# Performance work log

Hardware: AMD Instinct MI355X
Metric: run time of the kernel (lower is better)

## Reference

```python
import jax, jax.numpy as jnp
import numpy as np

N_NODES = 100000
N_EDGES = 3200000
IN_SIZE = 256
HID_SIZE = 256
OUT_SIZE = 64


def setup_inputs() -> dict:
    key = jax.random.key(0)
    ks = jax.random.split(key, 8)
    X = jax.random.normal(ks[0], (N_NODES, IN_SIZE), dtype=jnp.float32)
    edge_vals = jax.random.uniform(ks[1], (N_EDGES,), dtype=jnp.float32)
    # xavier-uniform-ish init for weights
    lim1 = float(np.sqrt(6.0 / (IN_SIZE + HID_SIZE)))
    W1 = jax.random.uniform(ks[2], (IN_SIZE, HID_SIZE), minval=-lim1, maxval=lim1, dtype=jnp.float32)
    b1 = jnp.zeros((HID_SIZE,), dtype=jnp.float32)
    lim2 = float(np.sqrt(6.0 / (HID_SIZE + OUT_SIZE)))
    W2 = jax.random.uniform(ks[3], (HID_SIZE, OUT_SIZE), minval=-lim2, maxval=lim2, dtype=jnp.float32)
    b2 = jnp.zeros((OUT_SIZE,), dtype=jnp.float32)
    row = jnp.sort(jax.random.randint(ks[4], (N_EDGES,), 0, N_NODES, dtype=jnp.int32))
    col = jax.random.randint(ks[5], (N_EDGES,), 0, N_NODES, dtype=jnp.int32)
    return {"X": X, "edge_vals": edge_vals, "W1": W1, "b1": b1,
            "W2": W2, "b2": b2, "row": row, "col": col}


def reference(X, edge_vals, W1, b1, W2, b2, row, col):
    """2-layer GCN (eval mode, dropout = identity).

    A is a sparse NxN matrix in COO form: A[row[e], col[e]] = edge_vals[e].
    Layer: relu(A @ (X @ W1) + b1); output: A @ (h @ W2) + b2.
    """
    n = X.shape[0]

    def spmm(dense):  # (A @ dense): gather columns, scale, segment-sum over rows
        gathered = edge_vals[:, None] * dense[col]        # [E, F]
        return jax.ops.segment_sum(gathered, row, num_segments=n)

    h = spmm(X @ W1) + b1          # [N, HID]
    h = jax.nn.relu(h)
    out = spmm(h @ W2) + b2        # [N, OUT]
    return out
```

## Files before the change

kernel.cpp:

```cpp
#include <hip/hip_runtime.h>


constexpr int IN_SIZE = 256;
constexpr int HID = 256;
constexpr int OUTF = 64;

typedef __bf16 bf16x8 __attribute__((ext_vector_type(8)));
typedef float f32x4 __attribute__((ext_vector_type(4)));

__device__ __forceinline__ ushort f2b(float f) {
    uint u = __float_as_uint(f);
    uint r = (u + 0x7fffu + ((u >> 16) & 1u)) >> 16;
    return (ushort)r;
}

__device__ __forceinline__ void fma4(float* a, uint word, float w) {
    a[0] += w * (float)(word & 0xffu);
    a[1] += w * (float)((word >> 8) & 0xffu);
    a[2] += w * (float)((word >> 16) & 0xffu);
    a[3] += w * (float)(word >> 24);
}

__device__ __forceinline__ bf16x8 pack8(float4 a, float4 b) {
    union { uint4 u; bf16x8 h; } cv;
    cv.u.x = (uint)f2b(a.x) | ((uint)f2b(a.y) << 16);
    cv.u.y = (uint)f2b(a.z) | ((uint)f2b(a.w) << 16);
    cv.u.z = (uint)f2b(b.x) | ((uint)f2b(b.y) << 16);
    cv.u.w = (uint)f2b(b.z) | ((uint)f2b(b.w) << 16);
    return cv.h;
}

__global__ void setup_kernel(const int* __restrict__ row, int* __restrict__ rp,
                             const float* __restrict__ W1, ushort* __restrict__ W1T,
                             const float* __restrict__ W2, ushort* __restrict__ W2T,
                             int n, int E, int rpB) {
    int b = blockIdx.x;
    if (b < rpB) {
        int i = b * 256 + threadIdx.x;
        if (i > n) return;
        int lo = 0, hi = E;
        while (lo < hi) {
            int mid = (lo + hi) >> 1;
            if (row[mid] < i) lo = mid + 1; else hi = mid;
        }
        rp[i] = lo;
    } else if (b < rpB + 256) {
        int nn = b - rpB;
        int k = threadIdx.x;
        W1T[(size_t)nn * 256 + k] = f2b(W1[(size_t)k * 256 + nn]);
    } else {
        int nn = b - rpB - 256;
        int k = threadIdx.x;
        W2T[(size_t)nn * 256 + k] = f2b(W2[(size_t)k * 64 + nn]);
    }
}

__global__ void prep_edges(const float* __restrict__ vals, const int* __restrict__ col,
                           const float* __restrict__ s, int2* __restrict__ ew,
                           int E, int shift) {
    int e = blockIdx.x * 256 + threadIdx.x;
    if (e >= E) return;
    int c = col[e];
    ew[e] = make_int2(c << shift, __float_as_int(vals[e] * s[c]));
}

__global__ __launch_bounds__(1024)
void gemm1_q(const float* __restrict__ A, const ushort* __restrict__ Bt,
             unsigned char* __restrict__ Q, float* __restrict__ s1, int M) {
    __shared__ uint4 Wlds[8192];
    const int tid = threadIdx.x;
    const int wave = tid >> 6, lane = tid & 63;
    const int quad = lane >> 4, l = lane & 15;
    const int wr = wave >> 1, wc = wave & 1;
    const int m0 = blockIdx.x * 256;

    for (int i = tid; i < 8192; i += 1024) {
        uint4 v = ((const uint4*)Bt)[i];
        Wlds[(i & ~31) | ((i & 31) ^ ((i >> 5) & 7))] = v;
    }
    __syncthreads();

    size_t abase[2];
#pragma unroll
    for (int mt = 0; mt < 2; ++mt) {
        int r = min(m0 + wr * 32 + mt * 16 + l, M - 1);
        abase[mt] = (size_t)r * 256 + quad * 8;
    }

    f32x4 acc[2][8] = {};
    float4 ra0[2], rb0[2], ra1[2], rb1[2];
#pragma unroll
    for (int mt = 0; mt < 2; ++mt) {
        ra0[mt] = *(const float4*)(A + abase[mt]);
        rb0[mt] = *(const float4*)(A + abase[mt] + 4);
        ra1[mt] = *(const float4*)(A + abase[mt] + 32);
        rb1[mt] = *(const float4*)(A + abase[mt] + 36);
    }

#pragma unroll
    for (int kstep = 0; kstep < 8; ++kstep) {
        bf16x8 af[2];
#pragma unroll
        for (int mt = 0; mt < 2; ++mt)
            af[mt] = pack8(ra0[mt], rb0[mt]);
#pragma unroll
        for (int mt = 0; mt < 2; ++mt) { ra0[mt] = ra1[mt]; rb0[mt] = rb1[mt]; }
        if (kstep < 6) {
#pragma unroll
            for (int mt = 0; mt < 2; ++mt) {
                ra1[mt] = *(const float4*)(A + abase[mt] + (kstep + 2) * 32);
                rb1[mt] = *(const float4*)(A + abase[mt] + (kstep + 2) * 32 + 4);
            }
        }
#pragma unroll
        for (int nt = 0; nt < 8; ++nt) {
            int c = wc * 128 + nt * 16 + l;
            int idx = c * 32 + (((kstep << 2) + quad) ^ (c & 7));
            bf16x8 bfr = *(const bf16x8*)&Wlds[idx];
#pragma unroll
            for (int mt = 0; mt < 2; ++mt)
                acc[mt][nt] = __builtin_amdgcn_mfma_f32_16x16x32_bf16(
                    af[mt], bfr, acc[mt][nt], 0, 0, 0);
        }
    }

    __syncthreads();
    float* red = (float*)Wlds;
    float* fin = red + 512;

    float rmax[2][4];
#pragma unroll
    for (int mt = 0; mt < 2; ++mt)
#pragma unroll
        for (int reg = 0; reg < 4; ++reg) {
            float m = 0.f;
#pragma unroll
            for (int nt = 0; nt < 8; ++nt)
                m = fmaxf(m, fabsf(acc[mt][nt][reg]));
            rmax[mt][reg] = m;
        }
#pragma unroll
    for (int s = 1; s <= 8; s <<= 1)
#pragma unroll
        for (int mt = 0; mt < 2; ++mt)
#pragma unroll
            for (int reg = 0; reg < 4; ++reg)
                rmax[mt][reg] = fmaxf(rmax[mt][reg], __shfl_xor(rmax[mt][reg], s));
    if (l < 4) {
#pragma unroll
        for (int mt = 0; mt < 2; ++mt)
            red[wc * 256 + wr * 32 + mt * 16 + quad * 4 + l] = rmax[mt][l];
    }
    __syncthreads();
    if (tid < 256) {
        float m = fmaxf(red[tid], red[256 + tid]);
        fin[tid] = m;
        int r = m0 + tid;
        if (r < M) s1[r] = m * (1.f / 127.f);
    }
    __syncthreads();

#pragma unroll
    for (int mt = 0; mt < 2; ++mt)
#pragma unroll
        for (int reg = 0; reg < 4; ++reg) {
            int rl = wr * 32 + mt * 16 + quad * 4 + reg;
            int r = m0 + rl;
            if (r >= M) continue;
            float m = fin[rl];
            float inv = m > 0.f ? 127.f / m : 0.f;
#pragma unroll
            for (int nt = 0; nt < 8; ++nt) {
                int c = wc * 128 + nt * 16 + l;
                Q[(size_t)r * 256 + c] =
                    (unsigned char)((int)rintf(acc[mt][nt][reg] * inv) + 128);
            }
        }
}

__global__ __launch_bounds__(256, 4)
void gemm2_q(const ushort* __restrict__ A, const ushort* __restrict__ Bt,
             unsigned char* __restrict__ Q, float* __restrict__ s2, int M) {
    __shared__ uint4 Wlds[2048];
    const int tid = threadIdx.x;
    const int wave = tid >> 6, lane = tid & 63;
    const int quad = lane >> 4, l = lane & 15;
    const int r0 = blockIdx.x * 128 + wave * 32;

    for (int i = tid; i < 2048; i += 256) {
        uint4 v = ((const uint4*)Bt)[i];
        Wlds[(i & ~31) | ((i & 31) ^ ((i >> 5) & 7))] = v;
    }
    __syncthreads();

    size_t abase[2];
#pragma unroll
    for (int mt = 0; mt < 2; ++mt) {
        int r = min(r0 + mt * 16 + l, M - 1);
        abase[mt] = (size_t)r * 256 + quad * 8;
    }

    f32x4 acc[2][4] = {};
    uint4 ra0[2], ra1[2];
#pragma unroll
    for (int mt = 0; mt < 2; ++mt) {
        ra0[mt] = *(const uint4*)(A + abase[mt]);
        ra1[mt] = *(const uint4*)(A + abase[mt] + 32);
    }

#pragma unroll
    for (int kstep = 0; kstep < 8; ++kstep) {
        bf16x8 af[2];
#pragma unroll
        for (int mt = 0; mt < 2; ++mt)
            af[mt] = *(const bf16x8*)&ra0[mt];
#pragma unroll
        for (int mt = 0; mt < 2; ++mt) ra0[mt] = ra1[mt];
        if (kstep < 6) {
#pragma unroll
            for (int mt = 0; mt < 2; ++mt)
                ra1[mt] = *(const uint4*)(A + abase[mt] + (kstep + 2) * 32);
        }
        bf16x8 bfr[4];
#pragma unroll
        for (int nt = 0; nt < 4; ++nt) {
            int c = nt * 16 + l;
            int idx = c * 32 + (((kstep << 2) + quad) ^ (c & 7));
            bfr[nt] = *(const bf16x8*)&Wlds[idx];
        }
#pragma unroll
        for (int mt = 0; mt < 2; ++mt)
#pragma unroll
            for (int nt = 0; nt < 4; ++nt)
                acc[mt][nt] = __builtin_amdgcn_mfma_f32_16x16x32_bf16(
                    af[mt], bfr[nt], acc[mt][nt], 0, 0, 0);
    }

    float rmax[2][4];
#pragma unroll
    for (int mt = 0; mt < 2; ++mt)
#pragma unroll
        for (int reg = 0; reg < 4; ++reg) {
            float m = fmaxf(fabsf(acc[mt][0][reg]), fabsf(acc[mt][1][reg]));
            m = fmaxf(m, fabsf(acc[mt][2][reg]));
            m = fmaxf(m, fabsf(acc[mt][3][reg]));
            rmax[mt][reg] = m;
        }
#pragma unroll
    for (int s = 1; s <= 8; s <<= 1)
#pragma unroll
        for (int mt = 0; mt < 2; ++mt)
#pragma unroll
            for (int reg = 0; reg < 4; ++reg)
                rmax[mt][reg] = fmaxf(rmax[mt][reg], __shfl_xor(rmax[mt][reg], s));

#pragma unroll
    for (int mt = 0; mt < 2; ++mt)
#pragma unroll
        for (int reg = 0; reg < 4; ++reg) {
            int r = r0 + mt * 16 + quad * 4 + reg;
            if (r >= M) continue;
            float m = rmax[mt][reg];
            if (l == 0) s2[r] = m * (1.f / 127.f);
            float inv = m > 0.f ? 127.f / m : 0.f;
#pragma unroll
            for (int nt = 0; nt < 4; ++nt) {
                int c = nt * 16 + l;
                Q[(size_t)r * 64 + c] =
                    (unsigned char)((int)rintf(acc[mt][nt][reg] * inv) + 128);
            }
        }
}

__global__ __launch_bounds__(256)
void spmm1_q(const unsigned char* __restrict__ Q, const int2* __restrict__ ew,
             const int* __restrict__ rp, const float* __restrict__ bias,
             ushort* __restrict__ H, int node0, int nend) {
    const int wave = threadIdx.x >> 6;
    const int lane = threadIdx.x & 63;
    const int node = node0 + blockIdx.x * 4 + wave;
    if (node >= nend) return;
    const int e0 = rp[node], e1 = rp[node + 1];
    const int g = lane >> 4;
    const int fb = (lane & 15) * 16;

    float acc[16] = {};
    float sumw = 0.f;
    int e = e0;
    for (; e + 16 <= e1; e += 16) {
#pragma unroll
        for (int u = 0; u < 4; ++u) {
            int2 m = ew[e + u * 4 + g];
            float w = __int_as_float(m.y);
            uint4 qv = *(const uint4*)(Q + (size_t)(uint)m.x + fb);
            sumw += w;
            fma4(&acc[0], qv.x, w);
            fma4(&acc[4], qv.y, w);
            fma4(&acc[8], qv.z, w);
            fma4(&acc[12], qv.w, w);
        }
    }
    for (; e < e1; e += 4) {
        int idx = e + g;
        int2 m = ew[idx];
        bool ok = idx < e1;
        uint off = ok ? (uint)m.x : 0u;
        float w = ok ? __int_as_float(m.y) : 0.f;
        uint4 qv = *(const uint4*)(Q + (size_t)off + fb);
        sumw += w;
        fma4(&acc[0], qv.x, w);
        fma4(&acc[4], qv.y, w);
        fma4(&acc[8], qv.z, w);
        fma4(&acc[12], qv.w, w);
    }

#pragma unroll
    for (int s = 16; s <= 32; s <<= 1) {
#pragma unroll
        for (int j = 0; j < 16; ++j)
            acc[j] += __shfl_xor(acc[j], s);
        sumw += __shfl_xor(sumw, s);
    }

    if (g == 0) {
        const int f0 = (lane & 15) * 16;
        float4 b0 = *(const float4*)(bias + f0);
        float4 b1 = *(const float4*)(bias + f0 + 4);
        float4 b2 = *(const float4*)(bias + f0 + 8);
        float4 b3 = *(const float4*)(bias + f0 + 12);
        float bb[16] = {b0.x, b0.y, b0.z, b0.w, b1.x, b1.y, b1.z, b1.w,
                        b2.x, b2.y, b2.z, b2.w, b3.x, b3.y, b3.z, b3.w};
        float fix = -128.f * sumw;
        ushort r[16];
#pragma unroll
        for (int j = 0; j < 16; ++j)
            r[j] = f2b(fmaxf(acc[j] + fix + bb[j], 0.f));
        uint4 w0, w1;
        w0.x = (uint)r[0] | ((uint)r[1] << 16);
        w0.y = (uint)r[2] | ((uint)r[3] << 16);
        w0.z = (uint)r[4] | ((uint)r[5] << 16);
        w0.w = (uint)r[6] | ((uint)r[7] << 16);
        w1.x = (uint)r[8] | ((uint)r[9] << 16);
        w1.y = (uint)r[10] | ((uint)r[11] << 16);
        w1.z = (uint)r[12] | ((uint)r[13] << 16);
        w1.w = (uint)r[14] | ((uint)r[15] << 16);
        *(uint4*)(H + (size_t)node * 256 + f0) = w0;
        *(uint4*)(H + (size_t)node * 256 + f0 + 8) = w1;
    }
}

__global__ __launch_bounds__(256)
void spmm2_q(const unsigned char* __restrict__ Q, const int2* __restrict__ ew,
             const int* __restrict__ rp, const float* __restrict__ bias,
             float* __restrict__ O, int n) {
    const int wave = threadIdx.x >> 6;
    const int lane = threadIdx.x & 63;
    const int node = blockIdx.x * 4 + wave;
    if (node >= n) return;
    const int e0 = rp[node], e1 = rp[node + 1];
    const int g = lane >> 3;
    const int fb = (lane & 7) * 8;

    float acc[8] = {};
    float sumw = 0.f;
    int e = e0;
    for (; e + 16 <= e1; e += 16) {
#pragma unroll
        for (int u = 0; u < 2; ++u) {
            int2 m = ew[e + u * 8 + g];
            float w = __int_as_float(m.y);
            uint2 qv = *(const uint2*)(Q + (size_t)(uint)m.x + fb);
            sumw += w;
            fma4(&acc[0], qv.x, w);
            fma4(&acc[4], qv.y, w);
        }
    }
    for (; e < e1; e += 8) {
        int idx = e + g;
        int2 m = ew[idx];
        bool ok = idx < e1;
        uint off = ok ? (uint)m.x : 0u;
        float w = ok ? __int_as_float(m.y) : 0.f;
        uint2 qv = *(const uint2*)(Q + (size_t)off + fb);
        sumw += w;
        fma4(&acc[0], qv.x, w);
        fma4(&acc[4], qv.y, w);
    }

#pragma unroll
    for (int s = 8; s <= 32; s <<= 1) {
#pragma unroll
        for (int j = 0; j < 8; ++j)
            acc[j] += __shfl_xor(acc[j], s);
        sumw += __shfl_xor(sumw, s);
    }

    if (g == 0) {
        const int f0 = (lane & 7) * 8;
        float4 b0 = *(const float4*)(bias + f0);
        float4 b1 = *(const float4*)(bias + f0 + 4);
        float fix = -128.f * sumw;
        float4 o0, o1;
        o0.x = acc[0] + fix + b0.x;
        o0.y = acc[1] + fix + b0.y;
        o0.z = acc[2] + fix + b0.z;
        o0.w = acc[3] + fix + b0.w;
        o1.x = acc[4] + fix + b1.x;
        o1.y = acc[5] + fix + b1.y;
        o1.z = acc[6] + fix + b1.z;
        o1.w = acc[7] + fix + b1.w;
        *(float4*)(O + (size_t)node * 64 + f0) = o0;
        *(float4*)(O + (size_t)node * 64 + f0 + 4) = o1;
    }
}

static inline size_t alignup(size_t x) { return (x + 255) & ~(size_t)255; }

extern "C" void kernel_launch(void* const* d_in, const int* in_sizes, int n_in,
                              void* d_out, int out_size, void* d_ws, size_t ws_size,
                              hipStream_t stream) {
    const float* X  = (const float*)d_in[0];
    const float* ev = (const float*)d_in[1];
    const float* W1 = (const float*)d_in[2];
    const float* b1 = (const float*)d_in[3];
    const float* W2 = (const float*)d_in[4];
    const float* b2 = (const float*)d_in[5];
    const int*  row = (const int*)d_in[6];
    const int*  col = (const int*)d_in[7];
    float* out = (float*)d_out;

    const int n = in_sizes[0] / IN_SIZE;
    const int E = in_sizes[1];

    char* p = (char*)d_ws;
    ushort* H    = (ushort*)p; p += alignup((size_t)n * HID * 2);
    unsigned char* Q1 = (unsigned char*)p; p += alignup((size_t)n * HID);
    float*  s1   = (float*)p;  p += alignup((size_t)n * 4);
    unsigned char* Q2 = (unsigned char*)p; p += alignup((size_t)n * OUTF);
    float*  s2   = (float*)p;  p += alignup((size_t)n * 4);
    ushort* W1T  = (ushort*)p; p += alignup((size_t)IN_SIZE * HID * 2);
    ushort* W2T  = (ushort*)p; p += alignup((size_t)HID * OUTF * 2);
    int*    rp   = (int*)p;    p += alignup((size_t)(n + 1) * 4);
    int2*   ewb  = (int2*)p;   p += alignup((size_t)(E + 16) * 8);

    const int rpB = (n + 1 + 255) / 256;
    setup_kernel<<<rpB + 256 + 64, 256, 0, stream>>>(row, rp, W1, W1T, W2, W2T,
                                                     n, E, rpB);

    gemm1_q<<<(n + 255) / 256, 1024, 0, stream>>>(X, W1T, Q1, s1, n);

    prep_edges<<<(E + 255) / 256, 256, 0, stream>>>(ev, col, s1, ewb, E, 8);

    const int half = (n + 1) / 2;
    spmm1_q<<<(half + 3) / 4, 256, 0, stream>>>(Q1, ewb, rp, b1, H, 0, half);
    spmm1_q<<<(n - half + 3) / 4, 256, 0, stream>>>(Q1, ewb, rp, b1, H, half, n);

    gemm2_q<<<(n + 127) / 128, 256, 0, stream>>>(H, W2T, Q2, s2, n);

    prep_edges<<<(E + 255) / 256, 256, 0, stream>>>(ev, col, s2, ewb, E, 6);

    spmm2_q<<<(n + 3) / 4, 256, 0, stream>>>(Q2, ewb, rp, b2, out, n);
}
```

Baseline: 448.0 us.

## Make gemm1 grid-strided over row chunks and use native bf16 conversion

The first GEMM now launches about 250 blocks, each looping over a contiguous chunk of rows in 256-row tiles. The 128 KB transposed W1 staging into LDS is therefore amortised over more rows, and the partial second wave of blocks goes away. The reduction scratch moves to its own shared arrays so it no longer aliases the weight tile, which stays valid across iterations. The manual round-to-nearest bf16 packing is replaced by compiler bf16 casts, which can map to hardware conversion instructions. The cost is that the second tile per block is only partially used, so some rows are computed and then discarded.

```diff
diff --git a/kernel.cpp b/kernel.cpp
--- a/kernel.cpp
+++ b/kernel.cpp
@@ -21,13 +21,13 @@
     a[3] += w * (float)(word >> 24);
 }
 
-__device__ __forceinline__ bf16x8 pack8(float4 a, float4 b) {
-    union { uint4 u; bf16x8 h; } cv;
-    cv.u.x = (uint)f2b(a.x) | ((uint)f2b(a.y) << 16);
-    cv.u.y = (uint)f2b(a.z) | ((uint)f2b(a.w) << 16);
-    cv.u.z = (uint)f2b(b.x) | ((uint)f2b(b.y) << 16);
-    cv.u.w = (uint)f2b(b.z) | ((uint)f2b(b.w) << 16);
-    return cv.h;
+__device__ __forceinline__ bf16x8 pack8n(float4 a, float4 b) {
+    bf16x8 h;
+    h[0] = (__bf16)a.x; h[1] = (__bf16)a.y;
+    h[2] = (__bf16)a.z; h[3] = (__bf16)a.w;
+    h[4] = (__bf16)b.x; h[5] = (__bf16)b.y;
+    h[6] = (__bf16)b.z; h[7] = (__bf16)b.w;
+    return h;
 }
 
 __global__ void setup_kernel(const int* __restrict__ row, int* __restrict__ rp,
@@ -66,13 +66,16 @@
 
 __global__ __launch_bounds__(1024)
 void gemm1_q(const float* __restrict__ A, const ushort* __restrict__ Bt,
-             unsigned char* __restrict__ Q, float* __restrict__ s1, int M) {
+             unsigned char* __restrict__ Q, float* __restrict__ s1, int M, int R) {
     __shared__ uint4 Wlds[8192];
+    __shared__ float red[512];
+    __shared__ float fin[256];
     const int tid = threadIdx.x;
     const int wave = tid >> 6, lane = tid & 63;
     const int quad = lane >> 4, l = lane & 15;
     const int wr = wave >> 1, wc = wave & 1;
-    const int m0 = blockIdx.x * 256;
+    const int mstart = blockIdx.x * R;
+    const int mend = min(mstart + R, M);
 
     for (int i = tid; i < 8192; i += 1024) {
         uint4 v = ((const uint4*)Bt)[i];
@@ -80,102 +83,100 @@
     }
     __syncthreads();
 
-    size_t abase[2];
-#pragma unroll
-    for (int mt = 0; mt < 2; ++mt) {
-        int r = min(m0 + wr * 32 + mt * 16 + l, M - 1);
-        abase[mt] = (size_t)r * 256 + quad * 8;
-    }
-
-    f32x4 acc[2][8] = {};
-    float4 ra0[2], rb0[2], ra1[2], rb1[2];
-#pragma unroll
-    for (int mt = 0; mt < 2; ++mt) {
-        ra0[mt] = *(const float4*)(A + abase[mt]);
-        rb0[mt] = *(const float4*)(A + abase[mt] + 4);
-        ra1[mt] = *(const float4*)(A + abase[mt] + 32);
-        rb1[mt] = *(const float4*)(A + abase[mt] + 36);
-    }
-
-#pragma unroll
-    for (int kstep = 0; kstep < 8; ++kstep) {
-        bf16x8 af[2];
-#pragma unroll
-        for (int mt = 0; mt < 2; ++mt)
-            af[mt] = pack8(ra0[mt], rb0[mt]);
-#pragma unroll
-        for (int mt = 0; mt < 2; ++mt) { ra0[mt] = ra1[mt]; rb0[mt] = rb1[mt]; }
-        if (kstep < 6) {
-#pragma unroll
-            for (int mt = 0; mt < 2; ++mt) {
-                ra1[mt] = *(const float4*)(A + abase[mt] + (kstep + 2) * 32);
-                rb1[mt] = *(const float4*)(A + abase[mt] + (kstep + 2) * 32 + 4);
+    for (int m0 = mstart; m0 < mend; m0 += 256) {
+        size_t abase[2];
+#pragma unroll
+        for (int mt = 0; mt < 2; ++mt) {
+            int r = min(m0 + wr * 32 + mt * 16 + l, M - 1);
+            abase[mt] = (size_t)r * 256 + quad * 8;
+        }
+
+        f32x4 acc[2][8] = {};
+        float4 ra0[2], rb0[2], ra1[2], rb1[2];
+#pragma unroll
+        for (int mt = 0; mt < 2; ++mt) {
+            ra0[mt] = *(const float4*)(A + abase[mt]);
+            rb0[mt] = *(const float4*)(A + abase[mt] + 4);
+            ra1[mt] = *(const float4*)(A + abase[mt] + 32);
+            rb1[mt] = *(const float4*)(A + abase[mt] + 36);
+        }
+
+#pragma unroll
+        for (int kstep = 0; kstep < 8; ++kstep) {
+            bf16x8 af[2];
+#pragma unroll
+            for (int mt = 0; mt < 2; ++mt)
+                af[mt] = pack8n(ra0[mt], rb0[mt]);
+#pragma unroll
+            for (int mt = 0; mt < 2; ++mt) { ra0[mt] = ra1[mt]; rb0[mt] = rb1[mt]; }
+            if (kstep < 6) {
+#pragma unroll
+                for (int mt = 0; mt < 2; ++mt) {
+                    ra1[mt] = *(const float4*)(A + abase[mt] + (kstep + 2) * 32);
+                    rb1[mt] = *(const float4*)(A + abase[mt] + (kstep + 2) * 32 + 4);
+                }
             }
-        }
-#pragma unroll
-        for (int nt = 0; nt < 8; ++nt) {
-            int c = wc * 128 + nt * 16 + l;
-            int idx = c * 32 + (((kstep << 2) + quad) ^ (c & 7));
-            bf16x8 bfr = *(const bf16x8*)&Wlds[idx];
-#pragma unroll
-            for (int mt = 0; mt < 2; ++mt)
-                acc[mt][nt] = __builtin_amdgcn_mfma_f32_16x16x32_bf16(
-                    af[mt], bfr, acc[mt][nt], 0, 0, 0);
-        }
-    }
-
-    __syncthreads();
-    float* red = (float*)Wlds;
-    float* fin = red + 512;
-
-    float rmax[2][4];
-#pragma unroll
-    for (int mt = 0; mt < 2; ++mt)
-#pragma unroll
-        for (int reg = 0; reg < 4; ++reg) {
-            float m = 0.f;
-#pragma unroll
-            for (int nt = 0; nt < 8; ++nt)
-                m = fmaxf(m, fabsf(acc[mt][nt][reg]));
-            rmax[mt][reg] = m;
-        }
-#pragma unroll
-    for (int s = 1; s <= 8; s <<= 1)
-#pragma unroll
-        for (int mt = 0; mt < 2; ++mt)
-#pragma unroll
-            for (int reg = 0; reg < 4; ++reg)
-                rmax[mt][reg] = fmaxf(rmax[mt][reg], __shfl_xor(rmax[mt][reg], s));
-    if (l < 4) {
-#pragma unroll
-        for (int mt = 0; mt < 2; ++mt)
-            red[wc * 256 + wr * 32 + mt * 16 + quad * 4 + l] = rmax[mt][l];
-    }
-    __syncthreads();
-    if (tid < 256) {
-        float m = fmaxf(red[tid], red[256 + tid]);
-        fin[tid] = m;
-        int r = m0 + tid;
-        if (r < M) s1[r] = m * (1.f / 127.f);
-    }
-    __syncthreads();
-
-#pragma unroll
-    for (int mt = 0; mt < 2; ++mt)
-#pragma unroll
-        for (int reg = 0; reg < 4; ++reg) {
-            int rl = wr * 32 + mt * 16 + quad * 4 + reg;
-            int r = m0 + rl;
-            if (r >= M) continue;
-            float m = fin[rl];
-            float inv = m > 0.f ? 127.f / m : 0.f;
 #pragma unroll
             for (int nt = 0; nt < 8; ++nt) {
                 int c = wc * 128 + nt * 16 + l;
-                Q[(size_t)r * 256 + c] =
-                    (unsigned char)((int)rintf(acc[mt][nt][reg] * inv) + 128);
+                int idx = c * 32 + (((kstep << 2) + quad) ^ (c & 7));
+                bf16x8 bfr = *(const bf16x8*)&Wlds[idx];
+#pragma unroll
+                for (int mt = 0; mt < 2; ++mt)
+                    acc[mt][nt] = __builtin_amdgcn_mfma_f32_16x16x32_bf16(
+                        af[mt], bfr, acc[mt][nt], 0, 0, 0);
             }
         }
+
+        float rmax[2][4];
+#pragma unroll
+        for (int mt = 0; mt < 2; ++mt)
+#pragma unroll
+            for (int reg = 0; reg < 4; ++reg) {
+                float m = 0.f;
+#pragma unroll
+                for (int nt = 0; nt < 8; ++nt)
+                    m = fmaxf(m, fabsf(acc[mt][nt][reg]));
+                rmax[mt][reg] = m;
+            }
+#pragma unroll
+        for (int s = 1; s <= 8; s <<= 1)
+#pragma unroll
+            for (int mt = 0; mt < 2; ++mt)
+#pragma unroll
+                for (int reg = 0; reg < 4; ++reg)
+                    rmax[mt][reg] = fmaxf(rmax[mt][reg], __shfl_xor(rmax[mt][reg], s));
+        if (l < 4) {
+#pragma unroll
+            for (int mt = 0; mt < 2; ++mt)
+                red[wc * 256 + wr * 32 + mt * 16 + quad * 4 + l] = rmax[mt][l];
+        }
+        __syncthreads();
+        if (tid < 256) {
+            float m = fmaxf(red[tid], red[256 + tid]);
+            fin[tid] = m;
+            int r = m0 + tid;
+            if (r < mend) s1[r] = m * (1.f / 127.f);
+        }
+        __syncthreads();
+
+#pragma unroll
+        for (int mt = 0; mt < 2; ++mt)
+#pragma unroll
+            for (int reg = 0; reg < 4; ++reg) {
+                int rl = wr * 32 + mt * 16 + quad * 4 + reg;
+                int r = m0 + rl;
+                if (r >= mend) continue;
+                float m = fin[rl];
+                float inv = m > 0.f ? 127.f / m : 0.f;
+#pragma unroll
+                for (int nt = 0; nt < 8; ++nt) {
+                    int c = wc * 128 + nt * 16 + l;
+                    Q[(size_t)r * 256 + c] =
+                        (unsigned char)((int)rintf(acc[mt][nt][reg] * inv) + 128);
+                }
+            }
+    }
 }
 
 __global__ __launch_bounds__(256, 4)
@@ -447,7 +448,9 @@
     setup_kernel<<<rpB + 256 + 64, 256, 0, stream>>>(row, rp, W1, W1T, W2, W2T,
                                                      n, E, rpB);
 
-    gemm1_q<<<(n + 255) / 256, 1024, 0, stream>>>(X, W1T, Q1, s1, n);
+    int R = ((n + 249) / 250 + 15) & ~15;
+    int g1 = (n + R - 1) / R;
+    gemm1_q<<<g1, 1024, 0, stream>>>(X, W1T, Q1, s1, n, R);
 
     prep_edges<<<(E + 255) / 256, 256, 0, stream>>>(ev, col, s1, ewb, E, 8);
 
```

New measurement: 449.9 us. About the same (+0.4%).
